# Kernel tuning notes

Hardware: AMD Instinct MI355X
Metric: run time of the kernel (lower is better)

Reference implementation:

```python
import jax, jax.numpy as jnp
import numpy as np

N_MFS = 2
N_FEATURES = 12
OUTPUT_DIM = 8
BATCH = 4096
N_RULES = N_MFS ** N_FEATURES  # 4096


def _rule_indices(n_features, n_mfs):
    r = np.arange(n_mfs ** n_features)
    # mixed-radix digits: indices[rule, feat] = (rule // n_mfs**feat) % n_mfs
    return np.stack([(r // (n_mfs ** f)) % n_mfs for f in range(n_features)], axis=1).astype(np.int32)


def setup_inputs() -> dict:
    key = jax.random.key(0)
    ks = jax.random.split(key, 6)
    x = jax.random.normal(ks[0], (BATCH, N_FEATURES), dtype=jnp.float32)
    center_base = jax.random.uniform(ks[1], (N_FEATURES, 1), minval=-1.0, maxval=0.0, dtype=jnp.float32)
    center_delta_raw = jax.random.normal(ks[2], (N_FEATURES, N_MFS - 1), dtype=jnp.float32) * 0.5
    width_raw = jax.random.normal(ks[3], (N_FEATURES, N_MFS), dtype=jnp.float32) * 0.5
    fan = N_RULES * N_FEATURES + OUTPUT_DIM
    limit = float(np.sqrt(6.0 / fan))
    consequent_p = jax.random.uniform(ks[4], (N_RULES, N_FEATURES, OUTPUT_DIM), minval=-limit, maxval=limit, dtype=jnp.float32)
    consequent_r = jnp.zeros((N_RULES, OUTPUT_DIM), dtype=jnp.float32)
    rule_mf_indices = jnp.asarray(_rule_indices(N_FEATURES, N_MFS))
    return {"x": x, "center_base": center_base, "center_delta_raw": center_delta_raw,
            "width_raw": width_raw, "consequent_p": consequent_p, "consequent_r": consequent_r,
            "rule_mf_indices": rule_mf_indices}


def reference(x, center_base, center_delta_raw, width_raw, consequent_p, consequent_r, rule_mf_indices):
    # ordered centers: base + cumsum(softplus(delta) + 1e-3)
    gaps = jax.nn.softplus(center_delta_raw) + 1e-3          # (F, M-1)
    offsets = jnp.cumsum(gaps, axis=1)
    centers = jnp.concatenate([center_base, center_base + offsets], axis=1)  # (F, M)
    widths = jax.nn.softplus(width_raw) + 1e-3                # (F, M)

    # Gaussian memberships: (B, F, M)
    d = x[:, :, None] - centers[None, :, :]
    memberships = jnp.exp(-jnp.square(d) / (2.0 * jnp.square(widths)[None, :, :]))

    # rule firing: product over features of gathered memberships (loop over small fixed F)
    firing = jnp.ones((x.shape[0], rule_mf_indices.shape[0]), dtype=x.dtype)  # (B, R)
    for f in range(memberships.shape[1]):
        firing = firing * memberships[:, f, :][:, rule_mf_indices[:, f]]
    firing_norm = firing / (jnp.sum(firing, axis=1, keepdims=True) + 1e-8)

    # per-rule linear consequents: (B, R, O)
    rule_outputs = jnp.einsum('bf,rfo->bro', x, consequent_p) + consequent_r[None, :, :]
    # weighted reduce over rules: (B, O)
    output = jnp.einsum('br,bro->bo', firing_norm, rule_outputs)
    return output
```

## Files before the change

### kernel.cpp

```cpp
#include <hip/hip_runtime.h>
#include <math.h>

#define NF 12
#define NB 4096
#define NR 4096
#define NO 8

typedef float f32x4v __attribute__((ext_vector_type(4)));
typedef short bf16x8 __attribute__((ext_vector_type(8)));
typedef unsigned int uint32x4 __attribute__((ext_vector_type(4)));

#define PT2_BYTES (128 * 8 * 512 * 2)
#define PARAMS_OFF PT2_BYTES
#define WS_NEED (PT2_BYTES + 2048)
#define PT_ELEMS (112 * 4096)

__device__ __forceinline__ float softplus_f(float v) {
    return fmaxf(v, 0.0f) + log1pf(__expf(-fabsf(v)));
}
__device__ __forceinline__ unsigned short f2bf(float f) {
    unsigned u = __float_as_uint(f);
    u += 0x7FFFu + ((u >> 16) & 1u);
    return (unsigned short)(u >> 16);
}
__device__ __forceinline__ unsigned cvt_pk_bf16(float a, float b) {
    unsigned r;
    asm("v_cvt_pk_bf16_f32 %0, %1, %2" : "=v"(r) : "v"(a), "v"(b));
    return r;
}

__device__ __forceinline__ void build_afrag(f32x4v lo0, f32x4v lo1, float hv,
                                            bf16x8& ah, bf16x8& al) {
    f32x4v hv4 = {hv, hv, hv, hv};
    f32x4v va = lo0 * hv4;
    f32x4v vb = lo1 * hv4;
    unsigned h0 = cvt_pk_bf16(va[0], va[1]), h1 = cvt_pk_bf16(va[2], va[3]);
    unsigned h2 = cvt_pk_bf16(vb[0], vb[1]), h3 = cvt_pk_bf16(vb[2], vb[3]);
    f32x4v hia = { __uint_as_float(h0 << 16), __uint_as_float(h0 & 0xFFFF0000u),
                   __uint_as_float(h1 << 16), __uint_as_float(h1 & 0xFFFF0000u) };
    f32x4v hib = { __uint_as_float(h2 << 16), __uint_as_float(h2 & 0xFFFF0000u),
                   __uint_as_float(h3 << 16), __uint_as_float(h3 & 0xFFFF0000u) };
    f32x4v ea = va - hia;
    f32x4v eb = vb - hib;
    unsigned q0 = cvt_pk_bf16(ea[0], ea[1]), q1 = cvt_pk_bf16(ea[2], ea[3]);
    unsigned q2 = cvt_pk_bf16(eb[0], eb[1]), q3 = cvt_pk_bf16(eb[2], eb[3]);
    union { uint32x4 u; bf16x8 v; } A, B;
    A.u = (uint32x4){h0, h1, h2, h3};
    B.u = (uint32x4){q0, q1, q2, q3};
    ah = A.v; al = B.v;
}

__global__ __launch_bounds__(512) void anfis_prep2(
    const float* __restrict__ cp, const float* __restrict__ cr,
    const float* __restrict__ center_base, const float* __restrict__ cdr,
    const float* __restrict__ wr,
    unsigned short* __restrict__ PT2, float* __restrict__ params,
    float* __restrict__ out_zero)
{
    __shared__ float s_cp[32 * 97];
    __shared__ float s_cr[32 * 8];
    const int kt = blockIdx.x;
    const int tid = threadIdx.x;

    if (kt < 64) out_zero[(size_t)kt * 512 + tid] = 0.0f;

    {
        const float4* cp4 = (const float4*)(cp + (size_t)kt * 32 * 96);
        for (int i = tid; i < 768; i += 512) {
            float4 v = cp4[i];
            int r = i / 24, c4 = i - r * 24;
            float* d = &s_cp[r * 97 + c4 * 4];
            d[0] = v.x; d[1] = v.y; d[2] = v.z; d[3] = v.w;
        }
        if (tid < 64) {
            float4 v = ((const float4*)(cr + (size_t)kt * 32 * 8))[tid];
            float* d = &s_cr[tid * 4];
            d[0] = v.x; d[1] = v.y; d[2] = v.z; d[3] = v.w;
        }
    }
    __syncthreads();

    const int g = tid >> 7, col = (tid >> 3) & 15, e = tid & 7;
    const int rr = g * 8 + e;
    #pragma unroll
    for (int j = 0; j < 8; ++j) {
        int n = j * 16 + col;
        float v = 0.f;
        if (n < 96) v = s_cp[rr * 97 + n];
        else if (n < 104) v = s_cr[rr * 8 + (n - 96)];
        PT2[(size_t)(kt * 8 + j) * 512 + tid] = f2bf(v);
    }

    if (kt == 0 && tid < NF) {
        float c0 = center_base[tid];
        float gap = softplus_f(cdr[tid]) + 1e-3f;
        float w0 = softplus_f(wr[tid * 2 + 0]) + 1e-3f;
        float w1 = softplus_f(wr[tid * 2 + 1]) + 1e-3f;
        params[tid * 4 + 0] = c0;
        params[tid * 4 + 1] = c0 + gap;
        params[tid * 4 + 2] = -0.5f / (w0 * w0);
        params[tid * 4 + 3] = -0.5f / (w1 * w1);
    }
}

__global__ __launch_bounds__(512, 4) void anfis_main6(
    const float* __restrict__ x,
    const unsigned short* __restrict__ PT2,
    const float* __restrict__ params,
    float* __restrict__ out)
{
    __shared__ float s_params[48];
    __shared__ float s_mf[64 * 24];
    __shared__ float s_prod[64 * 8];
    __shared__ float s_rcp[64];
    __shared__ float s_x[64 * 12];
    __shared__ float s_low[64 * 36];
    __shared__ float s_high[64 * 36];
    __shared__ __align__(16) unsigned char s_B[2 * 16384];

    const int tid = threadIdx.x;
    const int bid = blockIdx.x;
    const int ks = bid & 7;
    const int mt = bid >> 3;
    const int b0 = mt * 64;
    const int kt0 = ks * 16;

    const int w = tid >> 6, l = tid & 63;

    const unsigned char* ptBase = (const unsigned char*)PT2;
    #define STAGE(c, buf) do {                                                        \
        const unsigned char* gb = ptBase + ((size_t)(kt0 + 2 * (c)) << 13);           \
        unsigned char* lb = &s_B[(buf) * 16384];                                      \
        __builtin_amdgcn_global_load_lds(                                             \
            (const __attribute__((address_space(1))) void*)(gb + w * 1024 + l * 16),  \
            (__attribute__((address_space(3))) void*)(lb + w * 1024), 16, 0, 0);      \
        __builtin_amdgcn_global_load_lds(                                             \
            (const __attribute__((address_space(1))) void*)(gb + (8 + w) * 1024 + l * 16), \
            (__attribute__((address_space(3))) void*)(lb + (8 + w) * 1024), 16, 0, 0);\
    } while (0)

    STAGE(0, 0);
    STAGE(1, 1);

    if (tid < 192) {
        float4 v = ((const float4*)(x + (size_t)b0 * NF))[tid];
        float* d = &s_x[tid * 4];
        d[0] = v.x; d[1] = v.y; d[2] = v.z; d[3] = v.w;
    }
    if (tid >= 500) {
        int f = tid - 500;
        ((float4*)s_params)[f] = ((const float4*)params)[f];
    }
    __syncthreads();

    if (tid < 384) {
        int row = tid / 6, fp = tid - row * 6;
        float pr = 1.f;
        #pragma unroll
        for (int h = 0; h < 2; ++h) {
            int f = fp + h * 6;
            float xv = s_x[row * 12 + f];
            float4 pm = *(const float4*)&s_params[f * 4];
            float d0 = xv - pm.x, d1 = xv - pm.y;
            float m0 = __expf(d0 * d0 * pm.z);
            float m1 = __expf(d1 * d1 * pm.w);
            s_mf[row * 24 + f * 2 + 0] = m0;
            s_mf[row * 24 + f * 2 + 1] = m1;
            pr *= (m0 + m1);
        }
        s_prod[row * 8 + fp] = pr;
    }
    __syncthreads();
    if (tid < 64) {
        float S = 1.f;
        #pragma unroll
        for (int i = 0; i < 6; ++i) S *= s_prod[tid * 8 + i];
        s_rcp[tid] = 1.0f / (S + 1e-8f);
    }
    __syncthreads();

    {
        int row = tid >> 3, w8 = tid & 7;
        const float* mr = &s_mf[row * 24];
        #pragma unroll
        for (int i = 0; i < 4; ++i) {
            int ee = w8 * 4 + i;
            float p = 1.f;
            #pragma unroll
            for (int f = 0; f < 5; ++f) p *= mr[f * 2 + ((ee >> f) & 1)];
            s_low[row * 36 + ee] = p;
        }
        float rc = s_rcp[row];
        #pragma unroll
        for (int i = 0; i < 2; ++i) {
            int t = w8 * 2 + i;
            int ktg = kt0 + t;
            float p = rc;
            #pragma unroll
            for (int ff = 0; ff < 7; ++ff) p *= mr[(5 + ff) * 2 + ((ktg >> ff) & 1)];
            s_high[row * 36 + t] = p;
        }
    }
    __syncthreads();

    const int rg = w >> 1, cg = w & 1;
    const int col = l & 15, g = l >> 4;
    const int rowA = rg * 16 + col;

    f32x4v lo0 = *(const f32x4v*)&s_low[rowA * 36 + g * 8];
    f32x4v lo1 = *(const f32x4v*)&s_low[rowA * 36 + g * 8 + 4];
    const float* hptr = &s_high[rowA * 36];

    f32x4v acc[4];
    #pragma unroll
    for (int jj = 0; jj < 4; ++jj) acc[jj] = (f32x4v){0.f, 0.f, 0.f, 0.f};

    #pragma unroll 1
    for (int c = 0; c < 8; ++c) {
        const int cur = c & 1;
        if (c >= 1 && c + 1 < 8) STAGE(c + 1, cur ^ 1);
        #pragma unroll
        for (int kt2 = 0; kt2 < 2; ++kt2) {
            const unsigned char* fp8 = &s_B[cur * 16384 + kt2 * 8192 + cg * 4096 + l * 16];
            bf16x8 fr0 = *(const bf16x8*)(fp8);
            bf16x8 fr1 = *(const bf16x8*)(fp8 + 1024);
            bf16x8 fr2 = *(const bf16x8*)(fp8 + 2048);
            float hv = hptr[c * 2 + kt2];
            bf16x8 ah, al;
            build_afrag(lo0, lo1, hv, ah, al);
            acc[0] = __builtin_amdgcn_mfma_f32_16x16x32_bf16(ah, fr0, acc[0], 0, 0, 0);
            acc[0] = __builtin_amdgcn_mfma_f32_16x16x32_bf16(al, fr0, acc[0], 0, 0, 0);
            acc[1] = __builtin_amdgcn_mfma_f32_16x16x32_bf16(ah, fr1, acc[1], 0, 0, 0);
            acc[1] = __builtin_amdgcn_mfma_f32_16x16x32_bf16(al, fr1, acc[1], 0, 0, 0);
            acc[2] = __builtin_amdgcn_mfma_f32_16x16x32_bf16(ah, fr2, acc[2], 0, 0, 0);
            acc[2] = __builtin_amdgcn_mfma_f32_16x16x32_bf16(al, fr2, acc[2], 0, 0, 0);
            if (cg == 0) {
                bf16x8 fr3 = *(const bf16x8*)(fp8 + 3072);
                acc[3] = __builtin_amdgcn_mfma_f32_16x16x32_bf16(ah, fr3, acc[3], 0, 0, 0);
                acc[3] = __builtin_amdgcn_mfma_f32_16x16x32_bf16(al, fr3, acc[3], 0, 0, 0);
            }
        }
        __syncthreads();
    }
    #undef STAGE

    float* s_acc = (float*)s_B;
    #pragma unroll
    for (int jj = 0; jj < 4; ++jj) {
        if (cg == 0 || jj < 3) {
            int j = cg * 4 + jj;
            #pragma unroll
            for (int q = 0; q < 4; ++q)
                s_acc[(rg * 16 + g * 4 + q) * 116 + j * 16 + col] = acc[jj][q];
        }
    }
    __syncthreads();
    {
        const int row = tid >> 3, o = tid & 7;
        const float* ar = &s_acc[row * 116];
        float t = ar[96 + o];
        #pragma unroll
        for (int f = 0; f < NF; ++f) t = fmaf(s_x[row * 12 + f], ar[f * 8 + o], t);
        atomicAdd(&out[(size_t)(b0 + row) * NO + o], t);
    }
}

__global__ __launch_bounds__(256) void anfis_prep(
    const float* __restrict__ cp, const float* __restrict__ cr,
    unsigned short* __restrict__ PT)
{
    const int n = blockIdx.x;
    const int t = threadIdx.x;
    if (n < 96) {
        #pragma unroll
        for (int i = 0; i < 16; ++i) { int r = i * 256 + t; PT[n * 4096 + r] = f2bf(cp[r * 96 + n]); }
    } else if (n < 104) {
        const int o = n - 96;
        #pragma unroll
        for (int i = 0; i < 16; ++i) { int r = i * 256 + t; PT[n * 4096 + r] = f2bf(cr[r * 8 + o]); }
    } else {
        #pragma unroll
        for (int i = 0; i < 16; ++i) PT[n * 4096 + i * 256 + t] = 0;
    }
}

__global__ __launch_bounds__(512) void anfis_mfma(
    const float* __restrict__ x,
    const float* __restrict__ center_base,
    const float* __restrict__ center_delta_raw,
    const float* __restrict__ width_raw,
    const unsigned short* __restrict__ PT,
    float* __restrict__ out)
{
    __shared__ float s_mem[16 * 26];
    __shared__ float s_low[16 * 36];
    __shared__ float s_high[16 * 132];
    __shared__ float s_red[8 * 16 * 113];

    const int tid = threadIdx.x;
    const int b0 = blockIdx.x * 16;

    if (tid < 16) {
        const int b = b0 + tid;
        float S = 1.0f;
        #pragma unroll
        for (int f = 0; f < NF; ++f) {
            float cb  = center_base[f];
            float gap = softplus_f(center_delta_raw[f]) + 1e-3f;
            float c0 = cb, c1 = cb + gap;
            float w0 = softplus_f(width_raw[f * 2 + 0]) + 1e-3f;
            float w1 = softplus_f(width_raw[f * 2 + 1]) + 1e-3f;
            float xv = x[b * NF + f];
            float d0 = xv - c0, d1 = xv - c1;
            float m0 = __expf(-d0 * d0 / (2.0f * w0 * w0));
            float m1 = __expf(-d1 * d1 / (2.0f * w1 * w1));
            s_mem[tid * 26 + f * 2 + 0] = m0;
            s_mem[tid * 26 + f * 2 + 1] = m1;
            S *= (m0 + m1);
        }
        s_mem[tid * 26 + 24] = 1.0f / (S + 1e-8f);
    }
    __syncthreads();
    if (tid < 256) {
        const int row = tid >> 4, w16 = tid & 15;
        const float* mrow = &s_mem[row * 26];
        #pragma unroll
        for (int e = 2 * w16; e <= 2 * w16 + 1; ++e) {
            float p = 1.0f;
            #pragma unroll
            for (int f = 0; f < 5; ++f) p *= mrow[f * 2 + ((e >> f) & 1)];
            s_low[row * 36 + e] = p;
        }
        float rcp = mrow[24];
        #pragma unroll
        for (int i = 0; i < 8; ++i) {
            int e = w16 + 16 * i;
            float p = rcp;
            #pragma unroll
            for (int ff = 0; ff < 7; ++ff) p *= mrow[(5 + ff) * 2 + ((e >> ff) & 1)];
            s_high[row * 132 + e] = p;
        }
    }
    __syncthreads();

    const int w = tid >> 6;
    const int l = tid & 63;
    const int col = l & 15;
    const int g   = l >> 4;

    f32x4v lo0 = *(const f32x4v*)&s_low[col * 36 + g * 8];
    f32x4v lo1 = *(const f32x4v*)&s_low[col * 36 + g * 8 + 4];
    f32x4v hq0 = *(const f32x4v*)&s_high[col * 132 + w * 16 + 0];
    f32x4v hq1 = *(const f32x4v*)&s_high[col * 132 + w * 16 + 4];
    f32x4v hq2 = *(const f32x4v*)&s_high[col * 132 + w * 16 + 8];
    f32x4v hq3 = *(const f32x4v*)&s_high[col * 132 + w * 16 + 12];

    const unsigned short* pB = PT + (size_t)col * 4096 + g * 8 + w * 512;

    f32x4v acc[7];
    #pragma unroll
    for (int j = 0; j < 7; ++j) acc[j] = (f32x4v){0.f, 0.f, 0.f, 0.f};

    bf16x8 bf[2][7];
    #pragma unroll
    for (int j = 0; j < 7; ++j) bf[0][j] = *(const bf16x8*)(pB + j * 65536 + 0 * 32);
    #pragma unroll
    for (int j = 0; j < 7; ++j) bf[1][j] = *(const bf16x8*)(pB + j * 65536 + 1 * 32);

    #pragma unroll
    for (int s = 0; s < 16; ++s) {
        const float hv = (s < 4) ? hq0[s & 3] : (s < 8) ? hq1[s & 3]
                        : (s < 12) ? hq2[s & 3] : hq3[s & 3];
        bf16x8 ah, al;
        #pragma unroll
        for (int e = 0; e < 8; ++e) {
            float v = ((e < 4) ? lo0[e & 3] : lo1[e & 3]) * hv;
            unsigned short h = f2bf(v);
            float vh = __uint_as_float(((unsigned)h) << 16);
            ah[e] = (short)h;
            al[e] = (short)f2bf(v - vh);
        }
        #pragma unroll
        for (int j = 0; j < 7; ++j) {
            acc[j] = __builtin_amdgcn_mfma_f32_16x16x32_bf16(ah, bf[s & 1][j], acc[j], 0, 0, 0);
            acc[j] = __builtin_amdgcn_mfma_f32_16x16x32_bf16(al, bf[s & 1][j], acc[j], 0, 0, 0);
        }
        if (s + 2 < 16) {
            #pragma unroll
            for (int j = 0; j < 7; ++j)
                bf[s & 1][j] = *(const bf16x8*)(pB + j * 65536 + (s + 2) * 32);
        }
    }

    #pragma unroll
    for (int j = 0; j < 7; ++j)
        #pragma unroll
        for (int q = 0; q < 4; ++q)
            s_red[(w * 16 + g * 4 + q) * 113 + j * 16 + col] = acc[j][q];
    __syncthreads();

    if (tid < 128) {
        const int row = tid >> 3, o = tid & 7;
        float xr[NF];
        #pragma unroll
        for (int f = 0; f < NF; ++f) xr[f] = x[(b0 + row) * NF + f];
        float outv = 0.0f;
        #pragma unroll
        for (int ww = 0; ww < 8; ++ww) {
            const float* ar = &s_red[(ww * 16 + row) * 113];
            float t2 = ar[96 + o];
            #pragma unroll
            for (int f = 0; f < NF; ++f) t2 = fmaf(xr[f], ar[f * 8 + o], t2);
            outv += t2;
        }
        out[(b0 + row) * NO + o] = outv;
    }
}

extern "C" void kernel_launch(void* const* d_in, const int* in_sizes, int n_in,
                              void* d_out, int out_size, void* d_ws, size_t ws_size,
                              hipStream_t stream) {
    const float* x   = (const float*)d_in[0];
    const float* cb  = (const float*)d_in[1];
    const float* cdr = (const float*)d_in[2];
    const float* wr  = (const float*)d_in[3];
    const float* cp  = (const float*)d_in[4];
    const float* cr  = (const float*)d_in[5];
    float* out = (float*)d_out;

    if (ws_size >= (size_t)WS_NEED) {
        unsigned short* PT2 = (unsigned short*)d_ws;
        float* params = (float*)((char*)d_ws + PARAMS_OFF);
        anfis_prep2<<<128, 512, 0, stream>>>(cp, cr, cb, cdr, wr, PT2, params, out);
        anfis_main6<<<512, 512, 0, stream>>>(x, PT2, params, out);
    } else if (ws_size >= (size_t)PT_ELEMS * sizeof(unsigned short)) {
        unsigned short* PT = (unsigned short*)d_ws;
        anfis_prep<<<112, 256, 0, stream>>>(cp, cr, PT);
        anfis_mfma<<<NB / 16, 512, 0, stream>>>(x, cb, cdr, wr, PT, out);
    }
}
```

Before: 22.35 us.

## Factor high-feature firing out of MFMA operands and scale outputs per row

The A fragment is now built from the low-feature membership products only. It is split into bf16 hi/lo once before the K loop, rather than multiplied by the per-tile high factor and re-split every iteration. The high factor depends only on the batch row and K tile, so it is applied to each tile's MFMA result as a per-row vector multiply-accumulate, read from a transposed shared array. Waves are remapped to cover two row tiles by up to two column tiles, and the unused eighth column block is no longer staged. This removes per-iteration bf16 conversion work, at the cost of extra fp32 vector FMAs, zero-initialised MFMA chains and a different rounding order.

Measured after the change: 21.27 us, median of 3. 1.05x faster.

```diff
diff --git a/kernel.cpp b/kernel.cpp
--- a/kernel.cpp
+++ b/kernel.cpp
@@ -29,11 +29,8 @@
     return r;
 }
 
-__device__ __forceinline__ void build_afrag(f32x4v lo0, f32x4v lo1, float hv,
+__device__ __forceinline__ void build_split(f32x4v va, f32x4v vb,
                                             bf16x8& ah, bf16x8& al) {
-    f32x4v hv4 = {hv, hv, hv, hv};
-    f32x4v va = lo0 * hv4;
-    f32x4v vb = lo1 * hv4;
     unsigned h0 = cvt_pk_bf16(va[0], va[1]), h1 = cvt_pk_bf16(va[2], va[3]);
     unsigned h2 = cvt_pk_bf16(vb[0], vb[1]), h3 = cvt_pk_bf16(vb[2], vb[3]);
     f32x4v hia = { __uint_as_float(h0 << 16), __uint_as_float(h0 & 0xFFFF0000u),
@@ -103,7 +100,7 @@
     }
 }
 
-__global__ __launch_bounds__(512, 4) void anfis_main6(
+__global__ __launch_bounds__(512, 4) void anfis_main7(
     const float* __restrict__ x,
     const unsigned short* __restrict__ PT2,
     const float* __restrict__ params,
@@ -115,7 +112,7 @@
     __shared__ float s_rcp[64];
     __shared__ float s_x[64 * 12];
     __shared__ float s_low[64 * 36];
-    __shared__ float s_high[64 * 36];
+    __shared__ float s_highT[16 * 64];
     __shared__ __align__(16) unsigned char s_B[2 * 16384];
 
     const int tid = threadIdx.x;
@@ -129,14 +126,16 @@
 
     const unsigned char* ptBase = (const unsigned char*)PT2;
     #define STAGE(c, buf) do {                                                        \
-        const unsigned char* gb = ptBase + ((size_t)(kt0 + 2 * (c)) << 13);           \
-        unsigned char* lb = &s_B[(buf) * 16384];                                      \
-        __builtin_amdgcn_global_load_lds(                                             \
-            (const __attribute__((address_space(1))) void*)(gb + w * 1024 + l * 16),  \
-            (__attribute__((address_space(3))) void*)(lb + w * 1024), 16, 0, 0);      \
-        __builtin_amdgcn_global_load_lds(                                             \
-            (const __attribute__((address_space(1))) void*)(gb + (8 + w) * 1024 + l * 16), \
-            (__attribute__((address_space(3))) void*)(lb + (8 + w) * 1024), 16, 0, 0);\
+        if (w != 7) {                                                                 \
+            const unsigned char* gb = ptBase + ((size_t)(kt0 + 2 * (c)) << 13);       \
+            unsigned char* lb = &s_B[(buf) * 16384];                                  \
+            __builtin_amdgcn_global_load_lds(                                         \
+                (const __attribute__((address_space(1))) void*)(gb + w * 1024 + l * 16),  \
+                (__attribute__((address_space(3))) void*)(lb + w * 1024), 16, 0, 0);  \
+            __builtin_amdgcn_global_load_lds(                                         \
+                (const __attribute__((address_space(1))) void*)(gb + (8 + w) * 1024 + l * 16), \
+                (__attribute__((address_space(3))) void*)(lb + (8 + w) * 1024), 16, 0, 0);\
+        }                                                                             \
     } while (0)
 
     STAGE(0, 0);
@@ -198,22 +197,34 @@
             float p = rc;
             #pragma unroll
             for (int ff = 0; ff < 7; ++ff) p *= mr[(5 + ff) * 2 + ((ktg >> ff) & 1)];
-            s_high[row * 36 + t] = p;
-        }
-    }
-    __syncthreads();
-
-    const int rg = w >> 1, cg = w & 1;
+            s_highT[t * 64 + row] = p;
+        }
+    }
+    __syncthreads();
+
+    const int rp = w >> 2, cq = w & 3;
     const int col = l & 15, g = l >> 4;
-    const int rowA = rg * 16 + col;
-
-    f32x4v lo0 = *(const f32x4v*)&s_low[rowA * 36 + g * 8];
-    f32x4v lo1 = *(const f32x4v*)&s_low[rowA * 36 + g * 8 + 4];
-    const float* hptr = &s_high[rowA * 36];
-
-    f32x4v acc[4];
-    #pragma unroll
-    for (int jj = 0; jj < 4; ++jj) acc[jj] = (f32x4v){0.f, 0.f, 0.f, 0.f};
+    const int nj = (cq < 3) ? 2 : 1;
+    const int jb = cq * 2;
+
+    bf16x8 ah[2], al[2];
+    #pragma unroll
+    for (int i = 0; i < 2; ++i) {
+        int rowA = (rp * 2 + i) * 16 + col;
+        f32x4v lo0 = *(const f32x4v*)&s_low[rowA * 36 + g * 8];
+        f32x4v lo1 = *(const f32x4v*)&s_low[rowA * 36 + g * 8 + 4];
+        build_split(lo0, lo1, ah[i], al[i]);
+    }
+
+    f32x4v acc[2][2];
+    #pragma unroll
+    for (int i = 0; i < 2; ++i)
+        #pragma unroll
+        for (int jj = 0; jj < 2; ++jj) acc[i][jj] = (f32x4v){0.f, 0.f, 0.f, 0.f};
+    const f32x4v z4 = (f32x4v){0.f, 0.f, 0.f, 0.f};
+
+    const int hoff0 = (rp * 2 + 0) * 16 + g * 4;
+    const int hoff1 = (rp * 2 + 1) * 16 + g * 4;
 
     #pragma unroll 1
     for (int c = 0; c < 8; ++c) {
@@ -221,23 +232,27 @@
         if (c >= 1 && c + 1 < 8) STAGE(c + 1, cur ^ 1);
         #pragma unroll
         for (int kt2 = 0; kt2 < 2; ++kt2) {
-            const unsigned char* fp8 = &s_B[cur * 16384 + kt2 * 8192 + cg * 4096 + l * 16];
-            bf16x8 fr0 = *(const bf16x8*)(fp8);
-            bf16x8 fr1 = *(const bf16x8*)(fp8 + 1024);
-            bf16x8 fr2 = *(const bf16x8*)(fp8 + 2048);
-            float hv = hptr[c * 2 + kt2];
-            bf16x8 ah, al;
-            build_afrag(lo0, lo1, hv, ah, al);
-            acc[0] = __builtin_amdgcn_mfma_f32_16x16x32_bf16(ah, fr0, acc[0], 0, 0, 0);
-            acc[0] = __builtin_amdgcn_mfma_f32_16x16x32_bf16(al, fr0, acc[0], 0, 0, 0);
-            acc[1] = __builtin_amdgcn_mfma_f32_16x16x32_bf16(ah, fr1, acc[1], 0, 0, 0);
-            acc[1] = __builtin_amdgcn_mfma_f32_16x16x32_bf16(al, fr1, acc[1], 0, 0, 0);
-            acc[2] = __builtin_amdgcn_mfma_f32_16x16x32_bf16(ah, fr2, acc[2], 0, 0, 0);
-            acc[2] = __builtin_amdgcn_mfma_f32_16x16x32_bf16(al, fr2, acc[2], 0, 0, 0);
-            if (cg == 0) {
-                bf16x8 fr3 = *(const bf16x8*)(fp8 + 3072);
-                acc[3] = __builtin_amdgcn_mfma_f32_16x16x32_bf16(ah, fr3, acc[3], 0, 0, 0);
-                acc[3] = __builtin_amdgcn_mfma_f32_16x16x32_bf16(al, fr3, acc[3], 0, 0, 0);
+            const int t = c * 2 + kt2;
+            const unsigned char* base = &s_B[cur * 16384 + kt2 * 8192 + l * 16];
+            bf16x8 fr0 = *(const bf16x8*)(base + jb * 1024);
+            f32x4v hv0 = *(const f32x4v*)&s_highT[t * 64 + hoff0];
+            f32x4v hv1 = *(const f32x4v*)&s_highT[t * 64 + hoff1];
+            f32x4v q00, q10;
+            q00 = __builtin_amdgcn_mfma_f32_16x16x32_bf16(ah[0], fr0, z4, 0, 0, 0);
+            q00 = __builtin_amdgcn_mfma_f32_16x16x32_bf16(al[0], fr0, q00, 0, 0, 0);
+            q10 = __builtin_amdgcn_mfma_f32_16x16x32_bf16(ah[1], fr0, z4, 0, 0, 0);
+            q10 = __builtin_amdgcn_mfma_f32_16x16x32_bf16(al[1], fr0, q10, 0, 0, 0);
+            acc[0][0] += hv0 * q00;
+            acc[1][0] += hv1 * q10;
+            if (nj == 2) {
+                bf16x8 fr1 = *(const bf16x8*)(base + (jb + 1) * 1024);
+                f32x4v q01, q11;
+                q01 = __builtin_amdgcn_mfma_f32_16x16x32_bf16(ah[0], fr1, z4, 0, 0, 0);
+                q01 = __builtin_amdgcn_mfma_f32_16x16x32_bf16(al[0], fr1, q01, 0, 0, 0);
+                q11 = __builtin_amdgcn_mfma_f32_16x16x32_bf16(ah[1], fr1, z4, 0, 0, 0);
+                q11 = __builtin_amdgcn_mfma_f32_16x16x32_bf16(al[1], fr1, q11, 0, 0, 0);
+                acc[0][1] += hv0 * q01;
+                acc[1][1] += hv1 * q11;
             }
         }
         __syncthreads();
@@ -246,12 +261,15 @@
 
     float* s_acc = (float*)s_B;
     #pragma unroll
-    for (int jj = 0; jj < 4; ++jj) {
-        if (cg == 0 || jj < 3) {
-            int j = cg * 4 + jj;
-            #pragma unroll
-            for (int q = 0; q < 4; ++q)
-                s_acc[(rg * 16 + g * 4 + q) * 116 + j * 16 + col] = acc[jj][q];
+    for (int i = 0; i < 2; ++i) {
+        #pragma unroll
+        for (int jj = 0; jj < 2; ++jj) {
+            if (jj < nj) {
+                int j = jb + jj;
+                #pragma unroll
+                for (int q = 0; q < 4; ++q)
+                    s_acc[((rp * 2 + i) * 16 + g * 4 + q) * 116 + j * 16 + col] = acc[i][jj][q];
+            }
         }
     }
     __syncthreads();
@@ -432,7 +450,7 @@
         unsigned short* PT2 = (unsigned short*)d_ws;
         float* params = (float*)((char*)d_ws + PARAMS_OFF);
         anfis_prep2<<<128, 512, 0, stream>>>(cp, cr, cb, cdr, wr, PT2, params, out);
-        anfis_main6<<<512, 512, 0, stream>>>(x, PT2, params, out);
+        anfis_main7<<<512, 512, 0, stream>>>(x, PT2, params, out);
     } else if (ws_size >= (size_t)PT_ELEMS * sizeof(unsigned short)) {
         unsigned short* PT = (unsigned short*)d_ws;
         anfis_prep<<<112, 256, 0, stream>>>(cp, cr, PT);
```
